# Optimization experiments

Measured on AMD Instinct MI355X. Metric: run time of the kernel, lower is better.

Reference implementation:

```python
import jax, jax.numpy as jnp
import numpy as np
import itertools

B, N, C, D = 2, 150000, 64, 128  # samples, points/sample, channels, voxel grid extent
EPS = 1e-4  # BatchNormBlock eps
# 3x3x3 submanifold kernel offsets (27 taps)
OFFS = jnp.array(list(itertools.product((-1, 0, 1), repeat=3)), dtype=jnp.int32)  # [27,3]


def setup_inputs() -> dict:
    key = jax.random.key(0)
    k1, k2 = jax.random.split(key)
    rng = np.random.default_rng(0)
    # unique voxel coordinates per sample on a D^3 grid
    pos = np.stack([
        np.stack(np.unravel_index(rng.choice(D ** 3, size=N, replace=False), (D, D, D)), axis=-1)
        for _ in range(B)
    ]).astype(np.int32)  # [B,N,3]
    feats = jax.random.normal(k1, (B, N, C), jnp.float32)
    # 4 submanifold convs (2 residual blocks x 2 convs), fan-in scaled
    Ws = jax.random.normal(k2, (4, 27, C, C), jnp.float32) / np.sqrt(27 * C)
    gammas = jnp.ones((4, C), jnp.float32)
    betas = jnp.zeros((4, C), jnp.float32)
    return {"feats": feats, "Ws": Ws, "gammas": gammas, "betas": betas, "pos": jnp.asarray(pos)}


def _build_lut(pos_b):  # pos_b: [N,3] int32 -> dense hash grid [D^3] of point index or -1
    code = (pos_b[:, 0] * D + pos_b[:, 1]) * D + pos_b[:, 2]
    return jnp.full((D ** 3,), -1, jnp.int32).at[code].set(jnp.arange(N, dtype=jnp.int32))


def _subconv(x, lut_b, pos_b, W):
    # submanifold sparse conv: per kernel tap, gather neighbor features and GEMM
    # x:[N,C], lut_b:[D^3], pos_b:[N,3], W:[27,Cin,Cout]
    def step(acc, kw):
        d, Wk = kw
        npos = pos_b + d  # [N,3]
        valid = jnp.all((npos >= 0) & (npos < D), axis=-1)
        code = (npos[:, 0] * D + npos[:, 1]) * D + npos[:, 2]
        nidx = lut_b[jnp.where(valid, code, 0)]
        valid = valid & (nidx >= 0)
        g = jnp.where(valid[:, None], x[jnp.clip(nidx, 0, N - 1)], 0.0)  # [N,Cin]
        return acc + g @ Wk, None

    acc0 = jnp.zeros((x.shape[0], W.shape[-1]), x.dtype)
    acc, _ = jax.lax.scan(step, acc0, (OFFS, W))
    return acc


def _bn_relu(x, g, b):
    # BatchNormBlock (train mode, biased var over all concatenated points) + ReLU
    mu = x.mean(axis=(0, 1))
    var = jnp.mean(jnp.square(x - mu), axis=(0, 1))
    return jax.nn.relu((x - mu) * jax.lax.rsqrt(var + EPS) * g + b)


def reference(feats, Ws, gammas, betas, pos):
    lut = jax.vmap(_build_lut)(pos)  # [B, D^3]
    conv = jax.vmap(_subconv, in_axes=(0, 0, 0, None))
    x = feats
    for blk in range(2):  # conv_block_reps ResidualBlocks (NIN is Identity since nIn==nOut)
        out1 = x
        h = _bn_relu(x, gammas[2 * blk], betas[2 * blk])
        h = conv(h, lut, pos, Ws[2 * blk])
        h = _bn_relu(h, gammas[2 * blk + 1], betas[2 * blk + 1])
        out2 = conv(h, lut, pos, Ws[2 * blk + 1])
        x = out1 + out2
    return x
```

## Files before the change

kernel.cpp:

```cpp
#include <hip/hip_runtime.h>
#include <stdint.h>

#define DGRID 128
#define D3 (DGRID * DGRID * DGRID)
#define NBATCH 2
#define NPTS 150000
#define NROWS (NBATCH * NPTS)
#define NPAD 300032
#define ZROW NROWS
#define NCBLK (NPAD / 128)
#define EPSBN 1e-4f
#define SBLK 1024

typedef __attribute__((ext_vector_type(8))) short s16x8;
typedef __attribute__((ext_vector_type(4))) float f32x4;

static __device__ __forceinline__ uint32_t f2bf_rne(float f) {
  uint32_t b = __float_as_uint(f);
  return (b + 0x7FFFu + ((b >> 16) & 1u)) >> 16;
}

static __device__ __forceinline__ f32x4 mfma16(uint4 a, uint4 b, f32x4 c) {
  return __builtin_amdgcn_mfma_f32_16x16x32_bf16(
      __builtin_bit_cast(s16x8, a), __builtin_bit_cast(s16x8, b), c, 0, 0, 0);
}

__global__ void k_scatter(const int* __restrict__ pos, int* __restrict__ lut) {
  int g = blockIdx.x * blockDim.x + threadIdx.x;
  if (g >= NROWS) return;
  int b = g / NPTS;
  int i = g - b * NPTS;
  int x = pos[3 * g], y = pos[3 * g + 1], z = pos[3 * g + 2];
  lut[(size_t)b * D3 + (x * DGRID + y) * DGRID + z] = i;
}

__global__ void k_nbr(const int* __restrict__ pos, const int* __restrict__ lut,
                      int* __restrict__ nbr) {
  int g = blockIdx.x * blockDim.x + threadIdx.x;
  if (g >= NPAD) return;
  if (g >= NROWS) {
#pragma unroll
    for (int t = 0; t < 27; ++t) nbr[(size_t)t * NPAD + g] = ZROW;
    return;
  }
  int b = g / NPTS;
  int x = pos[3 * g], y = pos[3 * g + 1], z = pos[3 * g + 2];
  const int* L = lut + (size_t)b * D3;
#pragma unroll
  for (int t = 0; t < 27; ++t) {
    int nx = x + t / 9 - 1;
    int ny = y + (t / 3) % 3 - 1;
    int nz = z + t % 3 - 1;
    int v = ZROW;
    if ((unsigned)nx < DGRID && (unsigned)ny < DGRID && (unsigned)nz < DGRID) {
      int n = L[(nx * DGRID + ny) * DGRID + nz];
      if (n >= 0) v = b * NPTS + n;
    }
    nbr[(size_t)t * NPAD + g] = v;
  }
}

__global__ void k_wpack(const float* __restrict__ Ws, uint4* __restrict__ Wfrag) {
  int e = blockIdx.x * 256 + threadIdx.x;
  if (e >= 4 * 27 * 512) return;
  int lane = e & 63, nb = (e >> 6) & 3, s = (e >> 8) & 1, tt = e >> 9;
  int kb = s * 32 + (lane >> 4) * 8;
  int cout = nb * 16 + (lane & 15);
  const float* src = Ws + (size_t)tt * 4096;
  uint32_t p[4];
#pragma unroll
  for (int j = 0; j < 4; ++j) {
    uint32_t lo = f2bf_rne(src[(kb + 2 * j) * 64 + cout]);
    uint32_t hi = f2bf_rne(src[(kb + 2 * j + 1) * 64 + cout]);
    p[j] = (hi << 16) | lo;
  }
  uint4 o;
  o.x = p[0]; o.y = p[1]; o.z = p[2]; o.w = p[3];
  Wfrag[e] = o;
}

__global__ void k_stats1(const float* __restrict__ X, float* __restrict__ part) {
  __shared__ float s[512];
  int c = threadIdx.x & 63, q = threadIdx.x >> 6;
  float sm = 0.f, sq = 0.f;
  for (int r = blockIdx.x * 4 + q; r < NROWS; r += SBLK * 4) {
    float v = X[(size_t)r * 64 + c];
    sm += v;
    sq += v * v;
  }
  s[threadIdx.x] = sm;
  s[256 + threadIdx.x] = sq;
  __syncthreads();
  if (q == 0) {
    sm = s[c] + s[64 + c] + s[128 + c] + s[192 + c];
    sq = s[256 + c] + s[320 + c] + s[384 + c] + s[448 + c];
    part[blockIdx.x * 128 + c] = sm;
    part[blockIdx.x * 128 + 64 + c] = sq;
  }
}

__global__ void k_stats2(const float* __restrict__ part, int nblk,
                         const float* __restrict__ gamma, const float* __restrict__ beta,
                         float* __restrict__ chanp, int cid) {
  __shared__ float s[512];
  int c = threadIdx.x & 63, q = threadIdx.x >> 6;
  float sm = 0.f, sq = 0.f;
  for (int rb = q; rb < nblk; rb += 4) {
    sm += part[rb * 128 + c];
    sq += part[rb * 128 + 64 + c];
  }
  s[threadIdx.x] = sm;
  s[256 + threadIdx.x] = sq;
  __syncthreads();
  if (q == 0) {
    sm = s[c] + s[64 + c] + s[128 + c] + s[192 + c];
    sq = s[256 + c] + s[320 + c] + s[384 + c] + s[448 + c];
    float mean = sm / (float)NROWS;
    float var = sq / (float)NROWS - mean * mean;
    float a = gamma[cid * 64 + c] * rsqrtf(var + EPSBN);
    chanp[cid * 128 + c] = a;
    chanp[cid * 128 + 64 + c] = beta[cid * 64 + c] - mean * a;
  }
}

__global__ void k_hpass(const float* __restrict__ X, const float* __restrict__ chanp,
                        int cid, uint4* __restrict__ h) {
  int g = blockIdx.x * blockDim.x + threadIdx.x;
  if (g >= (NROWS + 1) * 8) return;
  if (g >= NROWS * 8) {
    h[g] = (uint4){0u, 0u, 0u, 0u};
    return;
  }
  int c0 = (g & 7) * 8;
  const float* cp = chanp + cid * 128;
  const float4 a0 = *(const float4*)(cp + c0);
  const float4 a1 = *(const float4*)(cp + c0 + 4);
  const float4 b0 = *(const float4*)(cp + 64 + c0);
  const float4 b1 = *(const float4*)(cp + 64 + c0 + 4);
  const float4 x0 = *(const float4*)(X + (size_t)g * 8);
  const float4 x1 = *(const float4*)(X + (size_t)g * 8 + 4);
  float v0 = fmaxf(fmaf(x0.x, a0.x, b0.x), 0.f);
  float v1 = fmaxf(fmaf(x0.y, a0.y, b0.y), 0.f);
  float v2 = fmaxf(fmaf(x0.z, a0.z, b0.z), 0.f);
  float v3 = fmaxf(fmaf(x0.w, a0.w, b0.w), 0.f);
  float v4 = fmaxf(fmaf(x1.x, a1.x, b1.x), 0.f);
  float v5 = fmaxf(fmaf(x1.y, a1.y, b1.y), 0.f);
  float v6 = fmaxf(fmaf(x1.z, a1.z, b1.z), 0.f);
  float v7 = fmaxf(fmaf(x1.w, a1.w, b1.w), 0.f);
  uint4 o;
  o.x = (f2bf_rne(v1) << 16) | f2bf_rne(v0);
  o.y = (f2bf_rne(v3) << 16) | f2bf_rne(v2);
  o.z = (f2bf_rne(v5) << 16) | f2bf_rne(v4);
  o.w = (f2bf_rne(v7) << 16) | f2bf_rne(v6);
  h[g] = o;
}

#define PH(T, WC, WN, AC, AN, NIA, NIL)                                     \
  {                                                                         \
    int tw = (T) + 1 <= 26 ? (T) + 1 : 26;                                  \
    const uint4* Wt = Wf + (size_t)tw * 512 + lane;                         \
    _Pragma("unroll") for (int i = 0; i < 8; i++) WN[i] = Wt[i * 64];       \
    int tn = (T) + 2 <= 26 ? (T) + 2 : 26;                                  \
    NIL[0] = nbp[(size_t)tn * NPAD];                                        \
    NIL[1] = nbp[(size_t)tn * NPAD + 16];                                   \
    {                                                                       \
      const uint4* hp0 = h + (size_t)NIA[0] * 8 + lkg;                      \
      const uint4* hp1 = h + (size_t)NIA[1] * 8 + lkg;                      \
      AN[0][0] = hp0[0]; AN[0][1] = hp0[4];                                 \
      AN[1][0] = hp1[0]; AN[1][1] = hp1[4];                                 \
    }                                                                       \
    _Pragma("unroll") for (int s = 0; s < 2; s++)                           \
      _Pragma("unroll") for (int rt = 0; rt < 2; rt++)                      \
        _Pragma("unroll") for (int nb = 0; nb < 4; nb++)                    \
          acc[rt][nb] = mfma16(AC[rt][s], WC[s * 4 + nb], acc[rt][nb]);     \
  }

__global__ __launch_bounds__(256, 3) void k_conv(
    const uint4* __restrict__ h, const uint4* __restrict__ Wf,
    const int* __restrict__ nbr, const float* __restrict__ res,
    float* __restrict__ out, float* __restrict__ part, int do_stats) {
  __shared__ float xp[4][16 * 68];
  __shared__ float sred[2][4][4][16];
  int tid = threadIdx.x, wv = tid >> 6, lane = tid & 63;
  int tbase = (blockIdx.x * 4 + wv) * 32;
  int lrow = lane & 15, lkg = lane >> 4;

  f32x4 acc[2][4];
#pragma unroll
  for (int i = 0; i < 2; i++)
#pragma unroll
    for (int j = 0; j < 4; j++) acc[i][j] = (f32x4){0.f, 0.f, 0.f, 0.f};

  const int* nbp = nbr + tbase + lrow;
  int n0[2], n1[2];
  uint4 w0[8], w1[8];
  uint4 a0[2][2], a1[2][2];

  int p0 = nbp[0], p1 = nbp[16];
  n1[0] = nbp[NPAD];
  n1[1] = nbp[NPAD + 16];
#pragma unroll
  for (int i = 0; i < 8; i++) w0[i] = Wf[i * 64 + lane];
  {
    const uint4* hp0 = h + (size_t)p0 * 8 + lkg;
    const uint4* hp1 = h + (size_t)p1 * 8 + lkg;
    a0[0][0] = hp0[0]; a0[0][1] = hp0[4];
    a0[1][0] = hp1[0]; a0[1][1] = hp1[4];
  }

  for (int t = 0; t < 26; t += 2) {
    PH(t, w0, w1, a0, a1, n1, n0)
    PH(t + 1, w1, w0, a1, a0, n0, n1)
  }
  PH(26, w0, w1, a0, a1, n1, n0)

  float smc[16], sqc[16];
#pragma unroll
  for (int j = 0; j < 16; j++) smc[j] = sqc[j] = 0.f;
  float* slab = xp[wv];
#pragma unroll 1
  for (int rt = 0; rt < 2; rt++) {
#pragma unroll
    for (int nb = 0; nb < 4; nb++)
#pragma unroll
      for (int r = 0; r < 4; r++)
        slab[(lkg * 4 + r) * 68 + nb * 16 + lrow] = acc[rt][nb][r];
    __syncthreads();
    int gr = tbase + rt * 16 + lrow;
    if (gr < NROWS) {
#pragma unroll
      for (int j = 0; j < 4; j++) {
        float4 vv = *(float4*)&slab[lrow * 68 + lkg * 16 + j * 4];
        size_t off = (size_t)gr * 64 + lkg * 16 + j * 4;
        if (res) {
          float4 rr = *(const float4*)(res + off);
          vv.x += rr.x; vv.y += rr.y; vv.z += rr.z; vv.w += rr.w;
        }
        *(float4*)(out + off) = vv;
        smc[j * 4 + 0] += vv.x; sqc[j * 4 + 0] += vv.x * vv.x;
        smc[j * 4 + 1] += vv.y; sqc[j * 4 + 1] += vv.y * vv.y;
        smc[j * 4 + 2] += vv.z; sqc[j * 4 + 2] += vv.z * vv.z;
        smc[j * 4 + 3] += vv.w; sqc[j * 4 + 3] += vv.w * vv.w;
      }
    }
    __syncthreads();
  }
  if (do_stats) {
#pragma unroll
    for (int j = 0; j < 16; j++) {
      smc[j] += __shfl_xor(smc[j], 1); sqc[j] += __shfl_xor(sqc[j], 1);
      smc[j] += __shfl_xor(smc[j], 2); sqc[j] += __shfl_xor(sqc[j], 2);
      smc[j] += __shfl_xor(smc[j], 4); sqc[j] += __shfl_xor(sqc[j], 4);
      smc[j] += __shfl_xor(smc[j], 8); sqc[j] += __shfl_xor(sqc[j], 8);
    }
    if (lrow == 0) {
#pragma unroll
      for (int j = 0; j < 16; j++) {
        sred[0][wv][lkg][j] = smc[j];
        sred[1][wv][lkg][j] = sqc[j];
      }
    }
    __syncthreads();
    if (tid < 64) {
      float s0 = 0.f, s1 = 0.f;
      int q = tid >> 4, c = tid & 15;
#pragma unroll
      for (int w = 0; w < 4; w++) {
        s0 += sred[0][w][q][c];
        s1 += sred[1][w][q][c];
      }
      part[blockIdx.x * 128 + tid] = s0;
      part[blockIdx.x * 128 + 64 + tid] = s1;
    }
  }
}

extern "C" void kernel_launch(void* const* d_in, const int* in_sizes, int n_in,
                              void* d_out, int out_size, void* d_ws, size_t ws_size,
                              hipStream_t stream) {
  const float* feats = (const float*)d_in[0];
  const float* Ws = (const float*)d_in[1];
  const float* gammas = (const float*)d_in[2];
  const float* betas = (const float*)d_in[3];
  const int* pos = (const int*)d_in[4];
  float* out = (float*)d_out;

  char* w = (char*)d_ws;
  auto alloc = [&](size_t b) {
    char* p = w;
    w += (b + 255) & ~(size_t)255;
    return p;
  };
  int* nbr = (int*)alloc((size_t)27 * NPAD * 4);
  uint4* Wfrag = (uint4*)alloc((size_t)4 * 27 * 512 * 16);
  float* part = (float*)alloc((size_t)NCBLK * 128 * 4);
  float* chanp = (float*)alloc((size_t)4 * 128 * 4);
  uint4* h = (uint4*)alloc((size_t)NPAD * 128);
  float* xbuf = (float*)alloc((size_t)NROWS * 64 * 4);
  char* reg0 = alloc((size_t)NROWS * 64 * 4);
  float* cbuf = (float*)reg0;
  int* lut = (int*)reg0;

  hipMemsetAsync(lut, 0xFF, (size_t)NBATCH * D3 * 4, stream);
  int gpts = (NROWS + 255) / 256;
  k_scatter<<<gpts, 256, 0, stream>>>(pos, lut);
  k_nbr<<<NPAD / 256, 256, 0, stream>>>(pos, lut, nbr);
  k_wpack<<<216, 256, 0, stream>>>(Ws, Wfrag);

  k_stats1<<<SBLK, 256, 0, stream>>>(feats, part);
  k_stats2<<<1, 256, 0, stream>>>(part, SBLK, gammas, betas, chanp, 0);
  k_hpass<<<9376, 256, 0, stream>>>(feats, chanp, 0, h);
  k_conv<<<NCBLK, 256, 0, stream>>>(h, Wfrag + 0 * 27 * 512, nbr, nullptr, cbuf, part, 1);

  k_stats2<<<1, 256, 0, stream>>>(part, NCBLK, gammas, betas, chanp, 1);
  k_hpass<<<9376, 256, 0, stream>>>(cbuf, chanp, 1, h);
  k_conv<<<NCBLK, 256, 0, stream>>>(h, Wfrag + 1 * 27 * 512, nbr, feats, xbuf, part, 1);

  k_stats2<<<1, 256, 0, stream>>>(part, NCBLK, gammas, betas, chanp, 2);
  k_hpass<<<9376, 256, 0, stream>>>(xbuf, chanp, 2, h);
  k_conv<<<NCBLK, 256, 0, stream>>>(h, Wfrag + 2 * 27 * 512, nbr, nullptr, cbuf, part, 1);

  k_stats2<<<1, 256, 0, stream>>>(part, NCBLK, gammas, betas, chanp, 3);
  k_hpass<<<9376, 256, 0, stream>>>(cbuf, chanp, 3, h);
  k_conv<<<NCBLK, 256, 0, stream>>>(h, Wfrag + 3 * 27 * 512, nbr, xbuf, out, part, 0);
}
```

Before: 1.439 ms.

## Reorder points by spatial cells and deepen conv gather pipeline to three stages

```diff
diff --git a/kernel.cpp b/kernel.cpp
--- a/kernel.cpp
+++ b/kernel.cpp
@@ -9,6 +9,7 @@
 #define NPAD 300032
 #define ZROW NROWS
 #define NCBLK (NPAD / 128)
+#define NCELLS 8192
 #define EPSBN 1e-4f
 #define SBLK 1024
 
@@ -34,18 +35,67 @@
   lut[(size_t)b * D3 + (x * DGRID + y) * DGRID + z] = i;
 }
 
-__global__ void k_nbr(const int* __restrict__ pos, const int* __restrict__ lut,
-                      int* __restrict__ nbr) {
+__global__ void k_cellcount(const int* __restrict__ pos, int* __restrict__ cnt) {
   int g = blockIdx.x * blockDim.x + threadIdx.x;
-  if (g >= NPAD) return;
-  if (g >= NROWS) {
-#pragma unroll
-    for (int t = 0; t < 27; ++t) nbr[(size_t)t * NPAD + g] = ZROW;
+  if (g >= NROWS) return;
+  int b = g / NPTS;
+  int cid = (b << 12) | ((pos[3 * g] >> 3) << 8) | ((pos[3 * g + 1] >> 3) << 4) |
+            (pos[3 * g + 2] >> 3);
+  atomicAdd(&cnt[cid], 1);
+}
+
+__global__ void k_scan(const int* __restrict__ cnt, int* __restrict__ cstart) {
+  __shared__ int s[1024];
+  int tid = threadIdx.x;
+  int e[8];
+  int sum = 0;
+#pragma unroll
+  for (int j = 0; j < 8; j++) {
+    int v = cnt[tid * 8 + j];
+    e[j] = sum;
+    sum += v;
+  }
+  s[tid] = sum;
+  __syncthreads();
+  for (int off = 1; off < 1024; off <<= 1) {
+    int t = (tid >= off) ? s[tid - off] : 0;
+    __syncthreads();
+    s[tid] += t;
+    __syncthreads();
+  }
+  int base = tid ? s[tid - 1] : 0;
+#pragma unroll
+  for (int j = 0; j < 8; j++) cstart[tid * 8 + j] = base + e[j];
+}
+
+__global__ void k_bucket(const int* __restrict__ pos, const int* __restrict__ cstart,
+                         int* __restrict__ fill, int* __restrict__ perm,
+                         int* __restrict__ iperm) {
+  int g = blockIdx.x * blockDim.x + threadIdx.x;
+  if (g >= NROWS) return;
+  int b = g / NPTS;
+  int cid = (b << 12) | ((pos[3 * g] >> 3) << 8) | ((pos[3 * g + 1] >> 3) << 4) |
+            (pos[3 * g + 2] >> 3);
+  int slot = cstart[cid] + atomicAdd(&fill[cid], 1);
+  perm[slot] = g;
+  iperm[g] = slot;
+}
+
+__global__ void k_nbr_s(const int* __restrict__ pos, const int* __restrict__ lut,
+                        const int* __restrict__ perm, const int* __restrict__ iperm,
+                        int* __restrict__ nbr) {
+  int s = blockIdx.x * blockDim.x + threadIdx.x;
+  if (s >= NPAD) return;
+  if (s >= NROWS) {
+#pragma unroll
+    for (int t = 0; t < 27; ++t) nbr[(size_t)t * NPAD + s] = ZROW;
     return;
   }
+  int g = perm[s];
   int b = g / NPTS;
   int x = pos[3 * g], y = pos[3 * g + 1], z = pos[3 * g + 2];
   const int* L = lut + (size_t)b * D3;
+  const int* ip = iperm + (size_t)b * NPTS;
 #pragma unroll
   for (int t = 0; t < 27; ++t) {
     int nx = x + t / 9 - 1;
@@ -54,9 +104,9 @@
     int v = ZROW;
     if ((unsigned)nx < DGRID && (unsigned)ny < DGRID && (unsigned)nz < DGRID) {
       int n = L[(nx * DGRID + ny) * DGRID + nz];
-      if (n >= 0) v = b * NPTS + n;
+      if (n >= 0) v = ip[n];
     }
-    nbr[(size_t)t * NPAD + g] = v;
+    nbr[(size_t)t * NPAD + s] = v;
   }
 }
 
@@ -124,21 +174,24 @@
 }
 
 __global__ void k_hpass(const float* __restrict__ X, const float* __restrict__ chanp,
-                        int cid, uint4* __restrict__ h) {
+                        int cid, const int* __restrict__ gperm, uint4* __restrict__ h) {
   int g = blockIdx.x * blockDim.x + threadIdx.x;
   if (g >= (NROWS + 1) * 8) return;
-  if (g >= NROWS * 8) {
+  int row = g >> 3;
+  if (row >= NROWS) {
     h[g] = (uint4){0u, 0u, 0u, 0u};
     return;
   }
+  int src = gperm ? gperm[row] : row;
   int c0 = (g & 7) * 8;
   const float* cp = chanp + cid * 128;
   const float4 a0 = *(const float4*)(cp + c0);
   const float4 a1 = *(const float4*)(cp + c0 + 4);
   const float4 b0 = *(const float4*)(cp + 64 + c0);
   const float4 b1 = *(const float4*)(cp + 64 + c0 + 4);
-  const float4 x0 = *(const float4*)(X + (size_t)g * 8);
-  const float4 x1 = *(const float4*)(X + (size_t)g * 8 + 4);
+  const float* Xr = X + (size_t)src * 64 + c0;
+  const float4 x0 = *(const float4*)Xr;
+  const float4 x1 = *(const float4*)(Xr + 4);
   float v0 = fmaxf(fmaf(x0.x, a0.x, b0.x), 0.f);
   float v1 = fmaxf(fmaf(x0.y, a0.y, b0.y), 0.f);
   float v2 = fmaxf(fmaf(x0.z, a0.z, b0.z), 0.f);
@@ -155,30 +208,31 @@
   h[g] = o;
 }
 
-#define PH(T, WC, WN, AC, AN, NIA, NIL)                                     \
+#define PH(T, WU, WL, AU, AL, NIU, NIL)                                     \
   {                                                                         \
     int tw = (T) + 1 <= 26 ? (T) + 1 : 26;                                  \
     const uint4* Wt = Wf + (size_t)tw * 512 + lane;                         \
-    _Pragma("unroll") for (int i = 0; i < 8; i++) WN[i] = Wt[i * 64];       \
-    int tn = (T) + 2 <= 26 ? (T) + 2 : 26;                                  \
-    NIL[0] = nbp[(size_t)tn * NPAD];                                        \
-    NIL[1] = nbp[(size_t)tn * NPAD + 16];                                   \
+    _Pragma("unroll") for (int i = 0; i < 8; i++) WL[i] = Wt[i * 64];       \
+    int tn = (T) + 4 <= 26 ? (T) + 4 : 26;                                  \
+    _Pragma("unroll") for (int rt = 0; rt < 2; rt++)                        \
+        NIL[rt] = nbp[(size_t)tn * NPAD + rt * 16];                         \
     {                                                                       \
-      const uint4* hp0 = h + (size_t)NIA[0] * 8 + lkg;                      \
-      const uint4* hp1 = h + (size_t)NIA[1] * 8 + lkg;                      \
-      AN[0][0] = hp0[0]; AN[0][1] = hp0[4];                                 \
-      AN[1][0] = hp1[0]; AN[1][1] = hp1[4];                                 \
+      const uint4* hp0 = h + (size_t)NIU[0] * 8 + lkg;                      \
+      const uint4* hp1 = h + (size_t)NIU[1] * 8 + lkg;                      \
+      AL[0][0] = hp0[0]; AL[0][1] = hp0[4];                                 \
+      AL[1][0] = hp1[0]; AL[1][1] = hp1[4];                                 \
     }                                                                       \
     _Pragma("unroll") for (int s = 0; s < 2; s++)                           \
       _Pragma("unroll") for (int rt = 0; rt < 2; rt++)                      \
         _Pragma("unroll") for (int nb = 0; nb < 4; nb++)                    \
-          acc[rt][nb] = mfma16(AC[rt][s], WC[s * 4 + nb], acc[rt][nb]);     \
-  }
-
-__global__ __launch_bounds__(256, 3) void k_conv(
+          acc[rt][nb] = mfma16(AU[rt][s], WU[s * 4 + nb], acc[rt][nb]);     \
+  }
+
+__global__ __launch_bounds__(256, 2) void k_conv(
     const uint4* __restrict__ h, const uint4* __restrict__ Wf,
     const int* __restrict__ nbr, const float* __restrict__ res,
-    float* __restrict__ out, float* __restrict__ part, int do_stats) {
+    const int* __restrict__ rperm, float* __restrict__ out,
+    const int* __restrict__ wperm, float* __restrict__ part, int do_stats) {
   __shared__ float xp[4][16 * 68];
   __shared__ float sred[2][4][4][16];
   int tid = threadIdx.x, wv = tid >> 6, lane = tid & 63;
@@ -192,27 +246,39 @@
     for (int j = 0; j < 4; j++) acc[i][j] = (f32x4){0.f, 0.f, 0.f, 0.f};
 
   const int* nbp = nbr + tbase + lrow;
-  int n0[2], n1[2];
-  uint4 w0[8], w1[8];
-  uint4 a0[2][2], a1[2][2];
-
-  int p0 = nbp[0], p1 = nbp[16];
-  n1[0] = nbp[NPAD];
-  n1[1] = nbp[NPAD + 16];
-#pragma unroll
-  for (int i = 0; i < 8; i++) w0[i] = Wf[i * 64 + lane];
+  int niA[2], niB[2], niC[2];
+  uint4 wA[8], wB[8], wC[8];
+  uint4 aA[2][2], aB[2][2], aC[2][2];
+
+  int p0[2], p1[2];
+#pragma unroll
+  for (int i = 0; i < 8; i++) wA[i] = Wf[i * 64 + lane];
+#pragma unroll
+  for (int rt = 0; rt < 2; rt++) p0[rt] = nbp[rt * 16];
+#pragma unroll
+  for (int rt = 0; rt < 2; rt++) p1[rt] = nbp[(size_t)NPAD + rt * 16];
+#pragma unroll
+  for (int rt = 0; rt < 2; rt++) niA[rt] = nbp[(size_t)2 * NPAD + rt * 16];
+#pragma unroll
+  for (int rt = 0; rt < 2; rt++) niB[rt] = nbp[(size_t)3 * NPAD + rt * 16];
   {
-    const uint4* hp0 = h + (size_t)p0 * 8 + lkg;
-    const uint4* hp1 = h + (size_t)p1 * 8 + lkg;
-    a0[0][0] = hp0[0]; a0[0][1] = hp0[4];
-    a0[1][0] = hp1[0]; a0[1][1] = hp1[4];
-  }
-
-  for (int t = 0; t < 26; t += 2) {
-    PH(t, w0, w1, a0, a1, n1, n0)
-    PH(t + 1, w1, w0, a1, a0, n0, n1)
-  }
-  PH(26, w0, w1, a0, a1, n1, n0)
+    const uint4* hp0 = h + (size_t)p0[0] * 8 + lkg;
+    const uint4* hp1 = h + (size_t)p0[1] * 8 + lkg;
+    aA[0][0] = hp0[0]; aA[0][1] = hp0[4];
+    aA[1][0] = hp1[0]; aA[1][1] = hp1[4];
+  }
+  {
+    const uint4* hp0 = h + (size_t)p1[0] * 8 + lkg;
+    const uint4* hp1 = h + (size_t)p1[1] * 8 + lkg;
+    aB[0][0] = hp0[0]; aB[0][1] = hp0[4];
+    aB[1][0] = hp1[0]; aB[1][1] = hp1[4];
+  }
+
+  for (int t = 0; t < 27; t += 3) {
+    PH(t, wA, wB, aA, aC, niA, niC)
+    PH(t + 1, wB, wC, aB, aA, niB, niA)
+    PH(t + 2, wC, wA, aC, aB, niC, niB)
+  }
 
   float smc[16], sqc[16];
 #pragma unroll
@@ -228,15 +294,17 @@
     __syncthreads();
     int gr = tbase + rt * 16 + lrow;
     if (gr < NROWS) {
+      int rowr = rperm ? rperm[gr] : gr;
+      int roww = wperm ? wperm[gr] : gr;
 #pragma unroll
       for (int j = 0; j < 4; j++) {
         float4 vv = *(float4*)&slab[lrow * 68 + lkg * 16 + j * 4];
-        size_t off = (size_t)gr * 64 + lkg * 16 + j * 4;
+        size_t cofs = (size_t)(lkg * 16 + j * 4);
         if (res) {
-          float4 rr = *(const float4*)(res + off);
+          float4 rr = *(const float4*)(res + (size_t)rowr * 64 + cofs);
           vv.x += rr.x; vv.y += rr.y; vv.z += rr.z; vv.w += rr.w;
         }
-        *(float4*)(out + off) = vv;
+        *(float4*)(out + (size_t)roww * 64 + cofs) = vv;
         smc[j * 4 + 0] += vv.x; sqc[j * 4 + 0] += vv.x * vv.x;
         smc[j * 4 + 1] += vv.y; sqc[j * 4 + 1] += vv.y * vv.y;
         smc[j * 4 + 2] += vv.z; sqc[j * 4 + 2] += vv.z * vv.z;
@@ -295,6 +363,11 @@
   uint4* Wfrag = (uint4*)alloc((size_t)4 * 27 * 512 * 16);
   float* part = (float*)alloc((size_t)NCBLK * 128 * 4);
   float* chanp = (float*)alloc((size_t)4 * 128 * 4);
+  int* perm = (int*)alloc((size_t)NPAD * 4);
+  int* iperm = (int*)alloc((size_t)NROWS * 4);
+  int* ccnt = (int*)alloc((size_t)NCELLS * 4);
+  int* cfill = (int*)alloc((size_t)NCELLS * 4);
+  int* cstart = (int*)alloc((size_t)NCELLS * 4);
   uint4* h = (uint4*)alloc((size_t)NPAD * 128);
   float* xbuf = (float*)alloc((size_t)NROWS * 64 * 4);
   char* reg0 = alloc((size_t)NROWS * 64 * 4);
@@ -302,25 +375,33 @@
   int* lut = (int*)reg0;
 
   hipMemsetAsync(lut, 0xFF, (size_t)NBATCH * D3 * 4, stream);
+  hipMemsetAsync(ccnt, 0, (size_t)NCELLS * 8, stream);
   int gpts = (NROWS + 255) / 256;
   k_scatter<<<gpts, 256, 0, stream>>>(pos, lut);
-  k_nbr<<<NPAD / 256, 256, 0, stream>>>(pos, lut, nbr);
+  k_cellcount<<<gpts, 256, 0, stream>>>(pos, ccnt);
+  k_scan<<<1, 1024, 0, stream>>>(ccnt, cstart);
+  k_bucket<<<gpts, 256, 0, stream>>>(pos, cstart, cfill, perm, iperm);
+  k_nbr_s<<<NPAD / 256, 256, 0, stream>>>(pos, lut, perm, iperm, nbr);
   k_wpack<<<216, 256, 0, stream>>>(Ws, Wfrag);
 
   k_stats1<<<SBLK, 256, 0, stream>>>(feats, part);
   k_stats2<<<1, 256, 0, stream>>>(part, SBLK, gammas, betas, chanp, 0);
-  k_hpass<<<9376, 256, 0, stream>>>(feats, chanp, 0, h);
-  k_conv<<<NCBLK, 256, 0, stream>>>(h, Wfrag + 0 * 27 * 512, nbr, nullptr, cbuf, part, 1);
+  k_hpass<<<9376, 256, 0, stream>>>(feats, chanp, 0, perm, h);
+  k_conv<<<NCBLK, 256, 0, stream>>>(h, Wfrag + 0 * 27 * 512, nbr, nullptr, nullptr,
+                                    cbuf, nullptr, part, 1);
 
   k_stats2<<<1, 256, 0, stream>>>(part, NCBLK, gammas, betas, chanp, 1);
-  k_hpass<<<9376, 256, 0, stream>>>(cbuf, chanp, 1, h);
-  k_conv<<<NCBLK, 256, 0, stream>>>(h, Wfrag + 1 * 27 * 512, nbr, feats, xbuf, part, 1);
+  k_hpass<<<9376, 256, 0, stream>>>(cbuf, chanp, 1, nullptr, h);
+  k_conv<<<NCBLK, 256, 0, stream>>>(h, Wfrag + 1 * 27 * 512, nbr, feats, perm,
+                                    xbuf, nullptr, part, 1);
 
   k_stats2<<<1, 256, 0, stream>>>(part, NCBLK, gammas, betas, chanp, 2);
-  k_hpass<<<9376, 256, 0, stream>>>(xbuf, chanp, 2, h);
-  k_conv<<<NCBLK, 256, 0, stream>>>(h, Wfrag + 2 * 27 * 512, nbr, nullptr, cbuf, part, 1);
+  k_hpass<<<9376, 256, 0, stream>>>(xbuf, chanp, 2, nullptr, h);
+  k_conv<<<NCBLK, 256, 0, stream>>>(h, Wfrag + 2 * 27 * 512, nbr, nullptr, nullptr,
+                                    cbuf, nullptr, part, 1);
 
   k_stats2<<<1, 256, 0, stream>>>(part, NCBLK, gammas, betas, chanp, 3);
-  k_hpass<<<9376, 256, 0, stream>>>(cbuf, chanp, 3, h);
-  k_conv<<<NCBLK, 256, 0, stream>>>(h, Wfrag + 3 * 27 * 512, nbr, xbuf, out, part, 0);
-}
+  k_hpass<<<9376, 256, 0, stream>>>(cbuf, chanp, 3, nullptr, h);
+  k_conv<<<NCBLK, 256, 0, stream>>>(h, Wfrag + 3 * 27 * 512, nbr, xbuf, nullptr,
+                                    out, perm, part, 0);
+}
```

Result: faster. 1.363 ms (-5.3%).
